# Optimization experiments

Hardware: AMD Instinct MI355X
Metric: run time of the kernel (lower is better)

Reference implementation:

```python
import jax, jax.numpy as jnp
import numpy as np

E, TOP_K = 8, 2
NEG_SLOPE = 0.01  # nn.LeakyReLU default


def setup_inputs() -> dict:
    key = jax.random.key(0)
    ks = jax.random.split(key, 8)
    B, S, H, F, R = 2, 4096, 2048, 8192, 16
    s_h = 1.0 / np.sqrt(H)
    s_f = 1.0 / np.sqrt(F)
    s_r = 1.0 / np.sqrt(R)
    return {
        "x": jax.random.normal(ks[0], (B, S, H), jnp.float32),
        "gate_w": jax.random.normal(ks[1], (E, H), jnp.float32) * s_h,
        "w1_A": jax.random.normal(ks[2], (E, R, H), jnp.float32) * s_h,
        "w1_B": jax.random.normal(ks[3], (E, F, R), jnp.float32) * s_r,
        "w2_A": jax.random.normal(ks[4], (E, R, F), jnp.float32) * s_f,
        "w2_B": jax.random.normal(ks[5], (E, H, R), jnp.float32) * s_r,
        "w3_A": jax.random.normal(ks[6], (E, R, H), jnp.float32) * s_h,
        "w3_B": jax.random.normal(ks[7], (E, F, R), jnp.float32) * s_r,
    }


def reference(x, gate_w, w1_A, w1_B, w2_A, w2_B, w3_A, w3_B):
    B, S, H = x.shape
    xs = x.reshape(-1, H)  # [T,H]
    # router: softmax in fp32, top-k, renormalize (matches torch code)
    logits = xs @ gate_w.T  # [T,E]
    probs = jax.nn.softmax(logits.astype(jnp.float32), axis=-1)
    rw, sel = jax.lax.top_k(probs, TOP_K)  # [T,K]
    rw = rw / jnp.sum(rw, axis=-1, keepdims=True)
    rw = rw.astype(x.dtype)
    # per-token per-expert combine weight (0 if expert not selected) [T,E]
    w_te = jnp.sum(jax.nn.one_hot(sel, E, dtype=rw.dtype) * rw[..., None], axis=1)
    out = jnp.zeros_like(xs)
    for e in range(E):  # small fixed expert loop; avoids [E,T,F] blowup
        h1 = (xs @ w1_A[e].T) @ w1_B[e].T          # [T,F]
        h3 = (xs @ w3_A[e].T) @ w3_B[e].T          # [T,F]
        h = jnp.where(h1 >= 0, h1, NEG_SLOPE * h1) * h3
        y = (h @ w2_A[e].T) @ w2_B[e].T            # [T,H]
        out = out + y * w_te[:, e:e + 1]
    return out.reshape(B, S, H), rw
```

## Files before the change

### kernel.cpp

```cpp
#include <hip/hip_runtime.h>
#include <hip/hip_bf16.h>

typedef __attribute__((ext_vector_type(8))) short short8;
typedef __attribute__((ext_vector_type(4))) float f32x4;
typedef __hip_bfloat16 bf16;

static constexpr int T_TOK = 8192;
static constexpr int HD    = 2048;
static constexpr int FD    = 8192;
static constexpr int NE    = 8;

#define MFMA16(a,b,c) __builtin_amdgcn_mfma_f32_16x16x32_bf16((a),(b),(c),0,0,0)

__global__ __launch_bounds__(256) void k_convert(
    const float* __restrict__ w1A, const float* __restrict__ w1B,
    const float* __restrict__ w2A, const float* __restrict__ w2B,
    const float* __restrict__ w3A, const float* __restrict__ w3B,
    bf16* __restrict__ bw1a3, bf16* __restrict__ bw1b, bf16* __restrict__ bw3b,
    bf16* __restrict__ bw2apk, bf16* __restrict__ bw2b, int* __restrict__ cnt)
{
  int i = blockIdx.x * 256 + threadIdx.x;
  if (blockIdx.x == 0 && threadIdx.x < 16) cnt[threadIdx.x] = 0;
  bw1b[i] = __float2bfloat16(w1B[i]);
  bw3b[i] = __float2bfloat16(w3B[i]);
  {
    int f = i & (FD - 1); int er = i >> 13; int e = er >> 4; int r = er & 15;
    int ft = f >> 5; int fo = f & 31;
    int sub = fo >> 4; int lg = (fo >> 2) & 3; int j = sub * 4 + (fo & 3);
    int lane = lg * 16 + r;
    bw2apk[((e * 256 + ft) * 64 + lane) * 8 + j] = __float2bfloat16(w2A[i]);
  }
  if (i < 256 * HD) {
    int h = i & (HD - 1); int nn = i >> 11; int e = nn >> 5; int rr = nn & 31;
    float v = (rr < 16) ? w1A[(e * 16 + rr) * HD + h] : w3A[(e * 16 + (rr - 16)) * HD + h];
    bw1a3[e * 65536 + (h >> 5) * 1024 + rr * 32 + (h & 31)] = __float2bfloat16(v);
  }
  if (i < NE * HD * 16) bw2b[i] = __float2bfloat16(w2B[i]);
}

__global__ __launch_bounds__(256) void k_router(
    const float* __restrict__ x, const float* __restrict__ gw,
    float* __restrict__ rw_out, int* __restrict__ cnt,
    int* __restrict__ tok, float* __restrict__ wl, int* __restrict__ selT,
    bf16* __restrict__ bx, int use_bx)
{
  int tid = threadIdx.x;
  int j = tid >> 4;
  int r = tid & 15;
  int t = blockIdx.x * 16 + j;

  const float4* xr = reinterpret_cast<const float4*>(x + (size_t)t * HD);
  float p[8];
#pragma unroll
  for (int e = 0; e < 8; e++) p[e] = 0.f;
#pragma unroll 4
  for (int it = 0; it < 32; it++) {
    float4 xv = xr[it * 16 + r];
#pragma unroll
    for (int e = 0; e < 8; e++) {
      float4 gv = reinterpret_cast<const float4*>(gw + e * HD)[it * 16 + r];
      p[e] += xv.x * gv.x + xv.y * gv.y + xv.z * gv.z + xv.w * gv.w;
    }
    if (use_bx) {
      alignas(8) bf16 tb[4];
      tb[0] = __float2bfloat16(xv.x); tb[1] = __float2bfloat16(xv.y);
      tb[2] = __float2bfloat16(xv.z); tb[3] = __float2bfloat16(xv.w);
      *reinterpret_cast<uint2*>(bx + (size_t)t * HD + (it * 16 + r) * 4) =
          *reinterpret_cast<const uint2*>(tb);
    }
  }
#pragma unroll
  for (int e = 0; e < 8; e++) {
#pragma unroll
    for (int m = 1; m <= 8; m <<= 1) p[e] += __shfl_xor(p[e], m);
  }

  __shared__ int   se0[16], se1[16];
  __shared__ float sw0[16], sw1[16];
  if (r == 0) {
    float m = -1e30f;
#pragma unroll
    for (int e = 0; e < 8; e++) m = fmaxf(m, p[e]);
    float q[8];
#pragma unroll
    for (int e = 0; e < 8; e++) q[e] = __expf(p[e] - m);
    int i0 = 0; float b0 = q[0];
#pragma unroll
    for (int e = 1; e < 8; e++) if (q[e] > b0) { b0 = q[e]; i0 = e; }
    int i1 = -1; float b1 = -1.f;
#pragma unroll
    for (int e = 0; e < 8; e++) if (e != i0 && q[e] > b1) { b1 = q[e]; i1 = e; }
    float inv = 1.f / (b0 + b1);
    float r0 = b0 * inv, r1 = b1 * inv;
    rw_out[t * 2 + 0] = r0; rw_out[t * 2 + 1] = r1;
    selT[t] = i0 | (i1 << 8);
    se0[j] = i0; se1[j] = i1; sw0[j] = r0; sw1[j] = r1;
  }
  __syncthreads();
  if (tid < 16) {
    int ls = tid, e = ls >> 1, slot = ls & 1;
    int c = 0;
#pragma unroll
    for (int jj = 0; jj < 16; jj++)
      c += (slot == 0 ? (se0[jj] == e) : (se1[jj] == e)) ? 1 : 0;
    if (c > 0) {
      int base = atomicAdd(&cnt[ls], c);
      int k = 0;
#pragma unroll
      for (int jj = 0; jj < 16; jj++) {
        bool hit = (slot == 0 ? (se0[jj] == e) : (se1[jj] == e));
        if (hit) {
          tok[ls * T_TOK + base + k] = blockIdx.x * 16 + jj;
          wl [ls * T_TOK + base + k] = (slot == 0 ? sw0[jj] : sw1[jj]);
          k++;
        }
      }
    }
  }
}

#define LDW(FT, B1, B3, W2) { \
    int f0_ = w * 512 + (FT) * 32; \
    _Pragma("unroll") \
    for (int sub = 0; sub < 2; sub++) { \
      int f_ = f0_ + sub * 16 + lm; \
      B1[sub] = *reinterpret_cast<const short8*>(w1e + f_ * 16 + r8); \
      B3[sub] = *reinterpret_cast<const short8*>(w3e + f_ * 16 + r8); \
    } \
    W2 = *reinterpret_cast<const short8*>(w2e + ((size_t)(f0_ >> 5) * 64 + l) * 8); }

#define CMP(B1, B3, W2) \
  _Pragma("unroll") \
  for (int m = 0; m < 2; m++) { \
    short8 hfrag; \
    _Pragma("unroll") \
    for (int sub = 0; sub < 2; sub++) { \
      f32x4 h1 = MFMA16(B1[sub], A1[m], zf); \
      f32x4 h3 = MFMA16(B3[sub], A3[m], zf); \
      _Pragma("unroll") \
      for (int i = 0; i < 4; i++) { \
        float a = h1[i]; \
        float hv = (a >= 0.f ? a : 0.01f * a) * h3[i]; \
        bf16 hb = __float2bfloat16(hv); \
        hfrag[sub * 4 + i] = *reinterpret_cast<short*>(&hb); \
      } \
    } \
    acc[m] = MFMA16(W2, hfrag, acc[m]); }

__global__ __launch_bounds__(1024) void k_fused(
    const float* __restrict__ x, const bf16* __restrict__ bx, int use_bx,
    const bf16* __restrict__ bw1a3,
    const bf16* __restrict__ bw1b, const bf16* __restrict__ bw3b,
    const bf16* __restrict__ bw2apk,
    const int* __restrict__ cnt, const int* __restrict__ tok,
    const float* __restrict__ wl, bf16* __restrict__ accbf)
{
  int b = blockIdx.x;
  int ls = ((b & 7) << 1) | ((b >> 3) & 1);
  int pt = b >> 4;
  int n = cnt[ls]; int p0 = pt * 32;
  if (p0 >= n) return;
  int e = ls >> 1;
  int tid = threadIdx.x;
  int w = tid >> 6, l = tid & 63, lm = l & 15, lg = l >> 4;

  __shared__ int toks[32];
  __shared__ __align__(16) bf16 aT[32 * 40];
  __shared__ __align__(16) char uni[16 * 32 * 17 * 4];
  float* part = reinterpret_cast<float*>(uni);
  float* red  = reinterpret_cast<float*>(uni);

  if (tid < 32) {
    int pos = p0 + tid; if (pos > n - 1) pos = n - 1;
    toks[tid] = tok[ls * T_TOK + pos];
  }
  __syncthreads();

  const f32x4 zf = {0.f, 0.f, 0.f, 0.f};
  {
    int tg = w >> 3, ks = w & 7;
    const bf16* be = bw1a3 + e * 65536 + ks * 8192 + lg * 8;
    f32x4 a0 = zf, a1 = zf;
    if (use_bx) {
      const bf16* xp = bx + (size_t)toks[tg * 16 + lm] * HD + ks * 256 + lg * 8;
#pragma unroll
      for (int kk2 = 0; kk2 < 8; kk2++) {
        short8 af = *reinterpret_cast<const short8*>(xp + kk2 * 32);
        short8 b0 = *reinterpret_cast<const short8*>(be + kk2 * 1024 + lm * 32);
        short8 b1 = *reinterpret_cast<const short8*>(be + kk2 * 1024 + (lm + 16) * 32);
        a0 = MFMA16(af, b0, a0);
        a1 = MFMA16(af, b1, a1);
      }
    } else {
      const float* xp = x + (size_t)toks[tg * 16 + lm] * HD + ks * 256 + lg * 8;
#pragma unroll
      for (int kk2 = 0; kk2 < 8; kk2++) {
        float4 v0 = *reinterpret_cast<const float4*>(xp + kk2 * 32);
        float4 v1 = *reinterpret_cast<const float4*>(xp + kk2 * 32 + 4);
        alignas(16) bf16 tmp[8];
        tmp[0] = __float2bfloat16(v0.x); tmp[1] = __float2bfloat16(v0.y);
        tmp[2] = __float2bfloat16(v0.z); tmp[3] = __float2bfloat16(v0.w);
        tmp[4] = __float2bfloat16(v1.x); tmp[5] = __float2bfloat16(v1.y);
        tmp[6] = __float2bfloat16(v1.z); tmp[7] = __float2bfloat16(v1.w);
        short8 af = *reinterpret_cast<const short8*>(tmp);
        short8 b0 = *reinterpret_cast<const short8*>(be + kk2 * 1024 + lm * 32);
        short8 b1 = *reinterpret_cast<const short8*>(be + kk2 * 1024 + (lm + 16) * 32);
        a0 = MFMA16(af, b0, a0);
        a1 = MFMA16(af, b1, a1);
      }
    }
#pragma unroll
    for (int i = 0; i < 4; i++) {
      int row = tg * 16 + lg * 4 + i;
      part[(ks * 32 + row) * 33 + lm]      = a0[i];
      part[(ks * 32 + row) * 33 + 16 + lm] = a1[i];
    }
  }
  __syncthreads();
  {
    int tokr = tid >> 5, c = tid & 31;
    float s = 0.f;
#pragma unroll
    for (int ks = 0; ks < 8; ks++) s += part[(ks * 32 + tokr) * 33 + c];
    aT[tokr * 40 + c] = __float2bfloat16(s);
  }
  __syncthreads();

  const short8 ZS = {0, 0, 0, 0, 0, 0, 0, 0};
  short8 A1[2], A3[2];
#pragma unroll
  for (int m = 0; m < 2; m++) {
    if (lg < 2) {
      A1[m] = *reinterpret_cast<const short8*>(&aT[(m * 16 + lm) * 40 + lg * 8]);
      A3[m] = *reinterpret_cast<const short8*>(&aT[(m * 16 + lm) * 40 + 16 + lg * 8]);
    } else { A1[m] = ZS; A3[m] = ZS; }
  }
  f32x4 acc[2];
  acc[0] = zf; acc[1] = zf;
  int r8 = (lg & 1) * 8;
  const bf16* w1e = bw1b   + (size_t)e * FD * 16;
  const bf16* w3e = bw3b   + (size_t)e * FD * 16;
  const bf16* w2e = bw2apk + (size_t)e * 131072;

  short8 b1A[2], b3A[2], w2A_;
  short8 b1B[2], b3B[2], w2B_;
  LDW(0, b1A, b3A, w2A_);
  for (int ft = 0; ft < 16; ft += 2) {
    LDW(ft + 1, b1B, b3B, w2B_);
    CMP(b1A, b3A, w2A_);
    if (ft + 2 < 16) { LDW(ft + 2, b1A, b3A, w2A_); }
    CMP(b1B, b3B, w2B_);
  }
#pragma unroll
  for (int m = 0; m < 2; m++)
#pragma unroll
    for (int i = 0; i < 4; i++)
      red[w * 544 + (m * 16 + lm) * 17 + lg * 4 + i] = acc[m][i];
  __syncthreads();
  if (tid < 512) {
    int p = tid >> 4, rh = tid & 15;
    int pos = p0 + p;
    if (pos < n) {
      float s = 0.f;
#pragma unroll
      for (int ww = 0; ww < 16; ww++) s += red[ww * 544 + p * 17 + rh];
      float wgt = wl[ls * T_TOK + pos];
      int t = toks[p];
      int sl = ls & 1;
      accbf[((size_t)t * 2 + sl) * 16 + rh] = __float2bfloat16(s * wgt);
    }
  }
}

__global__ __launch_bounds__(256) void k_out(
    const bf16* __restrict__ accbf, const bf16* __restrict__ bw2b,
    const int* __restrict__ selT, float* __restrict__ out)
{
  int tpt = blockIdx.x >> 3;
  int ht  = blockIdx.x & 7;
  int tid = threadIdx.x, w = tid >> 6, l = tid & 63, lm = l & 15, lg = l >> 4;
  int t0 = tpt * 64;
  int tA = t0 + w * 16 + lm;
  int r8 = (lg & 1) * 8;
  int slot = lg >> 1;
  short8 A = *reinterpret_cast<const short8*>(accbf + ((size_t)tA * 2 + slot) * 16 + r8);
  int sel = selT[tA];
  int my_e = (slot == 0) ? (sel & 255) : (sel >> 8);

  const short8 ZS = {0, 0, 0, 0, 0, 0, 0, 0};
  const f32x4 zf = {0.f, 0.f, 0.f, 0.f};
  f32x4 y[4][4];
#pragma unroll
  for (int nt = 0; nt < 4; nt++)
#pragma unroll
    for (int hi = 0; hi < 4; hi++) y[nt][hi] = zf;

#pragma unroll
  for (int e = 0; e < 8; e++) {
    short8 Ae = (my_e == e) ? A : ZS;
    const bf16* wbe = bw2b + (size_t)e * HD * 16;
#pragma unroll
    for (int nt = 0; nt < 4; nt++) {
#pragma unroll
      for (int hi = 0; hi < 4; hi++) {
        int h = ht * 256 + nt * 64 + hi * 16 + lm;
        short8 B = *reinterpret_cast<const short8*>(wbe + h * 16 + r8);
        y[nt][hi] = MFMA16(Ae, B, y[nt][hi]);
      }
    }
  }
#pragma unroll
  for (int nt = 0; nt < 4; nt++)
#pragma unroll
    for (int hi = 0; hi < 4; hi++)
#pragma unroll
      for (int i = 0; i < 4; i++)
        out[(size_t)(t0 + w * 16 + lg * 4 + i) * HD + ht * 256 + nt * 64 + hi * 16 + lm]
            = y[nt][hi][i];
}

extern "C" void kernel_launch(void* const* d_in, const int* in_sizes, int n_in,
                              void* d_out, int out_size, void* d_ws, size_t ws_size,
                              hipStream_t stream)
{
  const float* x   = (const float*)d_in[0];
  const float* gw  = (const float*)d_in[1];
  const float* w1A = (const float*)d_in[2];
  const float* w1B = (const float*)d_in[3];
  const float* w2A = (const float*)d_in[4];
  const float* w2B = (const float*)d_in[5];
  const float* w3A = (const float*)d_in[6];
  const float* w3B = (const float*)d_in[7];
  float* out = (float*)d_out;
  float* rw  = out + (size_t)T_TOK * HD;

  char* ws = (char*)d_ws;
  bf16*  bw1a3  = (bf16*)(ws + 0);
  bf16*  bw1b   = (bf16*)(ws + 1048576);
  bf16*  bw3b   = (bf16*)(ws + 3145728);
  bf16*  bw2apk = (bf16*)(ws + 5242880);
  bf16*  bw2b   = (bf16*)(ws + 7340032);
  bf16*  accbf  = (bf16*)(ws + 16252928);
  int*   cnt    = (int*) (ws + 16777216);
  int*   tok    = (int*) (ws + 16777472);
  float* wl     = (float*)(ws + 17301760);
  int*   selT   = (int*) (ws + 17825792);
  bf16*  bx     = (bf16*)(ws + 18874368);
  int use_bx = (ws_size >= (size_t)18874368 + 33554432) ? 1 : 0;

  k_convert<<<dim3(4096), dim3(256), 0, stream>>>(w1A, w1B, w2A, w2B, w3A, w3B,
                                                  bw1a3, bw1b, bw3b, bw2apk, bw2b, cnt);
  k_router <<<dim3(512),  dim3(256),  0, stream>>>(x, gw, rw, cnt, tok, wl, selT, bx, use_bx);
  k_fused  <<<dim3(4096), dim3(1024), 0, stream>>>(x, bx, use_bx, bw1a3, bw1b, bw3b, bw2apk,
                                                   cnt, tok, wl, accbf);
  k_out    <<<dim3(1024), dim3(256),  0, stream>>>(accbf, bw2b, selT, out);
}
```

Measured before the change: 153.7 us.

## Merge weight conversion with router and make fused MoE kernel persistent

Weight conversion and router are merged into one launch that dispatches on block index, and the counter reset becomes a memset. The fused expert kernel becomes persistent: 512 blocks of 512 threads loop over the 4096 work items. Each wave now covers twice the F range and twice the K slice, which halves the cross-wave reductions. The goal is to cut launch overhead, the cost of early-exiting blocks, and shared-memory reduction work. The cost is less parallelism per work item and an extra barrier per loop iteration.

```diff
diff --git a/kernel.cpp b/kernel.cpp
--- a/kernel.cpp
+++ b/kernel.cpp
@@ -12,42 +12,41 @@
 
 #define MFMA16(a,b,c) __builtin_amdgcn_mfma_f32_16x16x32_bf16((a),(b),(c),0,0,0)
 
-__global__ __launch_bounds__(256) void k_convert(
+__global__ __launch_bounds__(256) void k_prep(
     const float* __restrict__ w1A, const float* __restrict__ w1B,
     const float* __restrict__ w2A, const float* __restrict__ w2B,
     const float* __restrict__ w3A, const float* __restrict__ w3B,
     bf16* __restrict__ bw1a3, bf16* __restrict__ bw1b, bf16* __restrict__ bw3b,
-    bf16* __restrict__ bw2apk, bf16* __restrict__ bw2b, int* __restrict__ cnt)
-{
-  int i = blockIdx.x * 256 + threadIdx.x;
-  if (blockIdx.x == 0 && threadIdx.x < 16) cnt[threadIdx.x] = 0;
-  bw1b[i] = __float2bfloat16(w1B[i]);
-  bw3b[i] = __float2bfloat16(w3B[i]);
-  {
-    int f = i & (FD - 1); int er = i >> 13; int e = er >> 4; int r = er & 15;
-    int ft = f >> 5; int fo = f & 31;
-    int sub = fo >> 4; int lg = (fo >> 2) & 3; int j = sub * 4 + (fo & 3);
-    int lane = lg * 16 + r;
-    bw2apk[((e * 256 + ft) * 64 + lane) * 8 + j] = __float2bfloat16(w2A[i]);
-  }
-  if (i < 256 * HD) {
-    int h = i & (HD - 1); int nn = i >> 11; int e = nn >> 5; int rr = nn & 31;
-    float v = (rr < 16) ? w1A[(e * 16 + rr) * HD + h] : w3A[(e * 16 + (rr - 16)) * HD + h];
-    bw1a3[e * 65536 + (h >> 5) * 1024 + rr * 32 + (h & 31)] = __float2bfloat16(v);
-  }
-  if (i < NE * HD * 16) bw2b[i] = __float2bfloat16(w2B[i]);
-}
-
-__global__ __launch_bounds__(256) void k_router(
+    bf16* __restrict__ bw2apk, bf16* __restrict__ bw2b,
     const float* __restrict__ x, const float* __restrict__ gw,
     float* __restrict__ rw_out, int* __restrict__ cnt,
     int* __restrict__ tok, float* __restrict__ wl, int* __restrict__ selT,
     bf16* __restrict__ bx, int use_bx)
 {
   int tid = threadIdx.x;
+  if (blockIdx.x < 4096) {
+    int i = blockIdx.x * 256 + tid;
+    bw1b[i] = __float2bfloat16(w1B[i]);
+    bw3b[i] = __float2bfloat16(w3B[i]);
+    {
+      int f = i & (FD - 1); int er = i >> 13; int e = er >> 4; int r = er & 15;
+      int ft = f >> 5; int fo = f & 31;
+      int sub = fo >> 4; int lg = (fo >> 2) & 3; int j = sub * 4 + (fo & 3);
+      int lane = lg * 16 + r;
+      bw2apk[((e * 256 + ft) * 64 + lane) * 8 + j] = __float2bfloat16(w2A[i]);
+    }
+    if (i < 256 * HD) {
+      int h = i & (HD - 1); int nn = i >> 11; int e = nn >> 5; int rr = nn & 31;
+      float v = (rr < 16) ? w1A[(e * 16 + rr) * HD + h] : w3A[(e * 16 + (rr - 16)) * HD + h];
+      bw1a3[e * 65536 + (h >> 5) * 1024 + rr * 32 + (h & 31)] = __float2bfloat16(v);
+    }
+    if (i < NE * HD * 16) bw2b[i] = __float2bfloat16(w2B[i]);
+    return;
+  }
+  int rb = blockIdx.x - 4096;
   int j = tid >> 4;
   int r = tid & 15;
-  int t = blockIdx.x * 16 + j;
+  int t = rb * 16 + j;
 
   const float4* xr = reinterpret_cast<const float4*>(x + (size_t)t * HD);
   float p[8];
@@ -110,7 +109,7 @@
       for (int jj = 0; jj < 16; jj++) {
         bool hit = (slot == 0 ? (se0[jj] == e) : (se1[jj] == e));
         if (hit) {
-          tok[ls * T_TOK + base + k] = blockIdx.x * 16 + jj;
+          tok[ls * T_TOK + base + k] = rb * 16 + jj;
           wl [ls * T_TOK + base + k] = (slot == 0 ? sw0[jj] : sw1[jj]);
           k++;
         }
@@ -120,7 +119,7 @@
 }
 
 #define LDW(FT, B1, B3, W2) { \
-    int f0_ = w * 512 + (FT) * 32; \
+    int f0_ = w * 1024 + (FT) * 32; \
     _Pragma("unroll") \
     for (int sub = 0; sub < 2; sub++) { \
       int f_ = f0_ + sub * 16 + lm; \
@@ -147,7 +146,7 @@
     } \
     acc[m] = MFMA16(W2, hfrag, acc[m]); }
 
-__global__ __launch_bounds__(1024) void k_fused(
+__global__ __launch_bounds__(512) void k_fused(
     const float* __restrict__ x, const bf16* __restrict__ bx, int use_bx,
     const bf16* __restrict__ bw1a3,
     const bf16* __restrict__ bw1b, const bf16* __restrict__ bw3b,
@@ -155,120 +154,128 @@
     const int* __restrict__ cnt, const int* __restrict__ tok,
     const float* __restrict__ wl, bf16* __restrict__ accbf)
 {
-  int b = blockIdx.x;
-  int ls = ((b & 7) << 1) | ((b >> 3) & 1);
-  int pt = b >> 4;
-  int n = cnt[ls]; int p0 = pt * 32;
-  if (p0 >= n) return;
-  int e = ls >> 1;
   int tid = threadIdx.x;
   int w = tid >> 6, l = tid & 63, lm = l & 15, lg = l >> 4;
 
   __shared__ int toks[32];
   __shared__ __align__(16) bf16 aT[32 * 40];
-  __shared__ __align__(16) char uni[16 * 32 * 17 * 4];
+  __shared__ __align__(16) char uni[4352 * 4];
   float* part = reinterpret_cast<float*>(uni);
   float* red  = reinterpret_cast<float*>(uni);
 
-  if (tid < 32) {
-    int pos = p0 + tid; if (pos > n - 1) pos = n - 1;
-    toks[tid] = tok[ls * T_TOK + pos];
-  }
-  __syncthreads();
-
   const f32x4 zf = {0.f, 0.f, 0.f, 0.f};
-  {
-    int tg = w >> 3, ks = w & 7;
-    const bf16* be = bw1a3 + e * 65536 + ks * 8192 + lg * 8;
-    f32x4 a0 = zf, a1 = zf;
-    if (use_bx) {
-      const bf16* xp = bx + (size_t)toks[tg * 16 + lm] * HD + ks * 256 + lg * 8;
-#pragma unroll
-      for (int kk2 = 0; kk2 < 8; kk2++) {
-        short8 af = *reinterpret_cast<const short8*>(xp + kk2 * 32);
-        short8 b0 = *reinterpret_cast<const short8*>(be + kk2 * 1024 + lm * 32);
-        short8 b1 = *reinterpret_cast<const short8*>(be + kk2 * 1024 + (lm + 16) * 32);
-        a0 = MFMA16(af, b0, a0);
-        a1 = MFMA16(af, b1, a1);
-      }
-    } else {
-      const float* xp = x + (size_t)toks[tg * 16 + lm] * HD + ks * 256 + lg * 8;
-#pragma unroll
-      for (int kk2 = 0; kk2 < 8; kk2++) {
-        float4 v0 = *reinterpret_cast<const float4*>(xp + kk2 * 32);
-        float4 v1 = *reinterpret_cast<const float4*>(xp + kk2 * 32 + 4);
-        alignas(16) bf16 tmp[8];
-        tmp[0] = __float2bfloat16(v0.x); tmp[1] = __float2bfloat16(v0.y);
-        tmp[2] = __float2bfloat16(v0.z); tmp[3] = __float2bfloat16(v0.w);
-        tmp[4] = __float2bfloat16(v1.x); tmp[5] = __float2bfloat16(v1.y);
-        tmp[6] = __float2bfloat16(v1.z); tmp[7] = __float2bfloat16(v1.w);
-        short8 af = *reinterpret_cast<const short8*>(tmp);
-        short8 b0 = *reinterpret_cast<const short8*>(be + kk2 * 1024 + lm * 32);
-        short8 b1 = *reinterpret_cast<const short8*>(be + kk2 * 1024 + (lm + 16) * 32);
-        a0 = MFMA16(af, b0, a0);
-        a1 = MFMA16(af, b1, a1);
-      }
-    }
-#pragma unroll
-    for (int i = 0; i < 4; i++) {
-      int row = tg * 16 + lg * 4 + i;
-      part[(ks * 32 + row) * 33 + lm]      = a0[i];
-      part[(ks * 32 + row) * 33 + 16 + lm] = a1[i];
-    }
-  }
-  __syncthreads();
-  {
-    int tokr = tid >> 5, c = tid & 31;
-    float s = 0.f;
-#pragma unroll
-    for (int ks = 0; ks < 8; ks++) s += part[(ks * 32 + tokr) * 33 + c];
-    aT[tokr * 40 + c] = __float2bfloat16(s);
-  }
-  __syncthreads();
-
   const short8 ZS = {0, 0, 0, 0, 0, 0, 0, 0};
-  short8 A1[2], A3[2];
-#pragma unroll
-  for (int m = 0; m < 2; m++) {
-    if (lg < 2) {
-      A1[m] = *reinterpret_cast<const short8*>(&aT[(m * 16 + lm) * 40 + lg * 8]);
-      A3[m] = *reinterpret_cast<const short8*>(&aT[(m * 16 + lm) * 40 + 16 + lg * 8]);
-    } else { A1[m] = ZS; A3[m] = ZS; }
-  }
-  f32x4 acc[2];
-  acc[0] = zf; acc[1] = zf;
-  int r8 = (lg & 1) * 8;
-  const bf16* w1e = bw1b   + (size_t)e * FD * 16;
-  const bf16* w3e = bw3b   + (size_t)e * FD * 16;
-  const bf16* w2e = bw2apk + (size_t)e * 131072;
-
-  short8 b1A[2], b3A[2], w2A_;
-  short8 b1B[2], b3B[2], w2B_;
-  LDW(0, b1A, b3A, w2A_);
-  for (int ft = 0; ft < 16; ft += 2) {
-    LDW(ft + 1, b1B, b3B, w2B_);
-    CMP(b1A, b3A, w2A_);
-    if (ft + 2 < 16) { LDW(ft + 2, b1A, b3A, w2A_); }
-    CMP(b1B, b3B, w2B_);
-  }
-#pragma unroll
-  for (int m = 0; m < 2; m++)
-#pragma unroll
-    for (int i = 0; i < 4; i++)
-      red[w * 544 + (m * 16 + lm) * 17 + lg * 4 + i] = acc[m][i];
-  __syncthreads();
-  if (tid < 512) {
-    int p = tid >> 4, rh = tid & 15;
-    int pos = p0 + p;
-    if (pos < n) {
-      float s = 0.f;
-#pragma unroll
-      for (int ww = 0; ww < 16; ww++) s += red[ww * 544 + p * 17 + rh];
-      float wgt = wl[ls * T_TOK + pos];
-      int t = toks[p];
-      int sl = ls & 1;
-      accbf[((size_t)t * 2 + sl) * 16 + rh] = __float2bfloat16(s * wgt);
-    }
+
+  for (int item = blockIdx.x; item < 4096; item += 512) {
+    int ls = ((item & 7) << 1) | ((item >> 3) & 1);
+    int pt = item >> 4;
+    int n = cnt[ls]; int p0 = pt * 32;
+    if (p0 >= n) continue;
+    int e = ls >> 1;
+
+    if (tid < 32) {
+      int pos = p0 + tid; if (pos > n - 1) pos = n - 1;
+      toks[tid] = tok[ls * T_TOK + pos];
+    }
+    __syncthreads();
+
+    {
+      int tg = w >> 2, ks = w & 3;
+      const bf16* be = bw1a3 + e * 65536 + ks * 16384 + lg * 8;
+      f32x4 a0 = zf, a1 = zf;
+      if (use_bx) {
+        const bf16* xp = bx + (size_t)toks[tg * 16 + lm] * HD + ks * 512 + lg * 8;
+#pragma unroll 4
+        for (int kk2 = 0; kk2 < 16; kk2++) {
+          short8 af = *reinterpret_cast<const short8*>(xp + kk2 * 32);
+          short8 b0 = *reinterpret_cast<const short8*>(be + kk2 * 1024 + lm * 32);
+          short8 b1 = *reinterpret_cast<const short8*>(be + kk2 * 1024 + (lm + 16) * 32);
+          a0 = MFMA16(af, b0, a0);
+          a1 = MFMA16(af, b1, a1);
+        }
+      } else {
+        const float* xp = x + (size_t)toks[tg * 16 + lm] * HD + ks * 512 + lg * 8;
+#pragma unroll 4
+        for (int kk2 = 0; kk2 < 16; kk2++) {
+          float4 v0 = *reinterpret_cast<const float4*>(xp + kk2 * 32);
+          float4 v1 = *reinterpret_cast<const float4*>(xp + kk2 * 32 + 4);
+          alignas(16) bf16 tmp[8];
+          tmp[0] = __float2bfloat16(v0.x); tmp[1] = __float2bfloat16(v0.y);
+          tmp[2] = __float2bfloat16(v0.z); tmp[3] = __float2bfloat16(v0.w);
+          tmp[4] = __float2bfloat16(v1.x); tmp[5] = __float2bfloat16(v1.y);
+          tmp[6] = __float2bfloat16(v1.z); tmp[7] = __float2bfloat16(v1.w);
+          short8 af = *reinterpret_cast<const short8*>(tmp);
+          short8 b0 = *reinterpret_cast<const short8*>(be + kk2 * 1024 + lm * 32);
+          short8 b1 = *reinterpret_cast<const short8*>(be + kk2 * 1024 + (lm + 16) * 32);
+          a0 = MFMA16(af, b0, a0);
+          a1 = MFMA16(af, b1, a1);
+        }
+      }
+#pragma unroll
+      for (int i = 0; i < 4; i++) {
+        int row = tg * 16 + lg * 4 + i;
+        part[(ks * 32 + row) * 33 + lm]      = a0[i];
+        part[(ks * 32 + row) * 33 + 16 + lm] = a1[i];
+      }
+    }
+    __syncthreads();
+    {
+      int tokr = tid >> 4, c2 = (tid & 15) * 2;
+      float s0 = 0.f, s1 = 0.f;
+#pragma unroll
+      for (int ks = 0; ks < 4; ks++) {
+        s0 += part[(ks * 32 + tokr) * 33 + c2];
+        s1 += part[(ks * 32 + tokr) * 33 + c2 + 1];
+      }
+      aT[tokr * 40 + c2]     = __float2bfloat16(s0);
+      aT[tokr * 40 + c2 + 1] = __float2bfloat16(s1);
+    }
+    __syncthreads();
+
+    short8 A1[2], A3[2];
+#pragma unroll
+    for (int m = 0; m < 2; m++) {
+      if (lg < 2) {
+        A1[m] = *reinterpret_cast<const short8*>(&aT[(m * 16 + lm) * 40 + lg * 8]);
+        A3[m] = *reinterpret_cast<const short8*>(&aT[(m * 16 + lm) * 40 + 16 + lg * 8]);
+      } else { A1[m] = ZS; A3[m] = ZS; }
+    }
+    f32x4 acc[2];
+    acc[0] = zf; acc[1] = zf;
+    int r8 = (lg & 1) * 8;
+    const bf16* w1e = bw1b   + (size_t)e * FD * 16;
+    const bf16* w3e = bw3b   + (size_t)e * FD * 16;
+    const bf16* w2e = bw2apk + (size_t)e * 131072;
+
+    short8 b1A[2], b3A[2], w2A_;
+    short8 b1B[2], b3B[2], w2B_;
+    LDW(0, b1A, b3A, w2A_);
+    for (int ft = 0; ft < 32; ft += 2) {
+      LDW(ft + 1, b1B, b3B, w2B_);
+      CMP(b1A, b3A, w2A_);
+      if (ft + 2 < 32) { LDW(ft + 2, b1A, b3A, w2A_); }
+      CMP(b1B, b3B, w2B_);
+    }
+#pragma unroll
+    for (int m = 0; m < 2; m++)
+#pragma unroll
+      for (int i = 0; i < 4; i++)
+        red[w * 544 + (m * 16 + lm) * 17 + lg * 4 + i] = acc[m][i];
+    __syncthreads();
+    {
+      int p = tid >> 4, rh = tid & 15;
+      int pos = p0 + p;
+      if (pos < n) {
+        float s = 0.f;
+#pragma unroll
+        for (int ww = 0; ww < 8; ww++) s += red[ww * 544 + p * 17 + rh];
+        float wgt = wl[ls * T_TOK + pos];
+        int t = toks[p];
+        int sl = ls & 1;
+        accbf[((size_t)t * 2 + sl) * 16 + rh] = __float2bfloat16(s * wgt);
+      }
+    }
+    __syncthreads();
   }
 }
 
@@ -348,10 +355,11 @@
   bf16*  bx     = (bf16*)(ws + 18874368);
   int use_bx = (ws_size >= (size_t)18874368 + 33554432) ? 1 : 0;
 
-  k_convert<<<dim3(4096), dim3(256), 0, stream>>>(w1A, w1B, w2A, w2B, w3A, w3B,
-                                                  bw1a3, bw1b, bw3b, bw2apk, bw2b, cnt);
-  k_router <<<dim3(512),  dim3(256),  0, stream>>>(x, gw, rw, cnt, tok, wl, selT, bx, use_bx);
-  k_fused  <<<dim3(4096), dim3(1024), 0, stream>>>(x, bx, use_bx, bw1a3, bw1b, bw3b, bw2apk,
-                                                   cnt, tok, wl, accbf);
-  k_out    <<<dim3(1024), dim3(256),  0, stream>>>(accbf, bw2b, selT, out);
+  hipMemsetAsync(cnt, 0, 64, stream);
+  k_prep <<<dim3(4608), dim3(256),  0, stream>>>(w1A, w1B, w2A, w2B, w3A, w3B,
+                                                 bw1a3, bw1b, bw3b, bw2apk, bw2b,
+                                                 x, gw, rw, cnt, tok, wl, selT, bx, use_bx);
+  k_fused<<<dim3(512),  dim3(512),  0, stream>>>(x, bx, use_bx, bw1a3, bw1b, bw3b, bw2apk,
+                                                 cnt, tok, wl, accbf);
+  k_out  <<<dim3(1024), dim3(256),  0, stream>>>(accbf, bw2b, selT, out);
 }
```

Result: slower. 170.3 us (+10.8%).
